# Kernel tuning notes

Measured on AMD Instinct MI355X. Metric: run time of the kernel, lower is better.

Reference implementation:

```python
import jax, jax.numpy as jnp
import numpy as np

B, N, T, F_IN, F_OUT = 4, 2048, 12, 32, 32
ALPHA = 0.2  # leaky relu negative slope
NEG_INF = -9e15


def setup_inputs() -> dict:
    key = jax.random.key(0)
    k = jax.random.split(key, 6)
    x = jax.random.normal(k[0], (B, N, T, F_IN), dtype=jnp.float32)
    adj = jax.random.randint(k[1], (N, N), 0, 2, dtype=jnp.int32)
    W = jax.random.normal(k[2], (T * F_IN, T * F_OUT), dtype=jnp.float32) * 0.05
    a = jax.random.normal(k[3], (2 * T * F_OUT, 1), dtype=jnp.float32) * 0.05
    conv_w = jax.random.normal(k[4], (T, T, 3), dtype=jnp.float32) * 0.1  # (out_ch, in_ch, k)
    conv_b = jnp.zeros((T,), dtype=jnp.float32)
    return {"x": x, "adj": adj, "W": W, "a": a, "conv_w": conv_w, "conv_b": conv_b}


def reference(x, adj, W, a, conv_w, conv_b):
    Bz, Nn, Tt, Fi = x.shape
    Fo = W.shape[1] // Tt
    # temporal conv: channels = timesteps, length = nodes*features
    xt = x.transpose(0, 2, 1, 3).reshape(Bz, Tt, Nn * Fi)  # (B,T,L)
    xt = jax.lax.conv_general_dilated(
        xt, conv_w, window_strides=(1,), padding=[(1, 1)],
        dimension_numbers=("NCH", "OIH", "NCH")) + conv_b[None, :, None]
    xt = xt.reshape(Bz, Tt, Nn, Fi).transpose(0, 2, 1, 3).reshape(Bz, Nn, Tt * Fi)
    Wh = xt @ W  # (B, N, T*Fo)
    # e[b,i,j] = leakyrelu(Wh[b,i].a1 + Wh[b,j].a2)  -- avoids O(N^2 * 2F) concat
    a1 = a[: Tt * Fo, 0]
    a2 = a[Tt * Fo:, 0]
    f1 = Wh @ a1  # (B, N)
    f2 = Wh @ a2  # (B, N)
    e = jax.nn.leaky_relu(f1[:, :, None] + f2[:, None, :], negative_slope=ALPHA)
    e = jnp.where(adj[None, :, :] > 0, e, NEG_INF)
    attn = jax.nn.softmax(e, axis=-1)  # (B, N, N); dropout omitted (eval mode)
    h_prime = attn @ Wh  # (B, N, T*Fo)
    return jax.nn.elu(h_prime).reshape(Bz, Nn, Tt, Fo)
```

## Files before the change

kernel.cpp:

```cpp
#include <hip/hip_runtime.h>

using short8 = __attribute__((ext_vector_type(8))) short;
using f32x4  = __attribute__((ext_vector_type(4))) float;
using f32x16 = __attribute__((ext_vector_type(16))) float;

__device__ __forceinline__ unsigned short f2bf(float f) {
  unsigned u = __float_as_uint(f);
  u += 0x7fffu + ((u >> 16) & 1u);
  return (unsigned short)(u >> 16);
}

__global__ __launch_bounds__(256) void pack_w_kernel(const float* __restrict__ W,
                                                     unsigned short* __restrict__ wtp) {
  const int f = blockIdx.x * 4 + (threadIdx.x >> 6);
  const int l = threadIdx.x & 63;
  const int kk = f / 24, ct = f % 24;
  const int il = l & 15, kg = l >> 4;
  const float* src = W + (size_t)(kk * 32 + kg * 8) * 384 + ct * 16 + il;
  short8 v;
#pragma unroll
  for (int e = 0; e < 8; ++e) v[e] = (short)f2bf(src[(size_t)e * 384]);
  *reinterpret_cast<short8*>((char*)wtp + ((size_t)f << 10) + l * 16) = v;
}

__global__ __launch_bounds__(256) void adjmask_kernel(const int* __restrict__ adj,
                                                      unsigned* __restrict__ adjm,
                                                      float* __restrict__ f12) {
  if (blockIdx.x < 64) f12[blockIdx.x * 256 + threadIdx.x] = 0.f;
  const int wv = (blockIdx.x << 2) + (threadIdx.x >> 6);
  const int lane = threadIdx.x & 63;
  const int row = wv >> 5, j0 = (wv & 31) << 6;
  unsigned long long mask = __ballot(adj[(size_t)row * 2048 + j0 + lane] > 0);
  if (lane == 0) {
    adjm[row * 64 + (j0 >> 5)]     = (unsigned)mask;
    adjm[row * 64 + (j0 >> 5) + 1] = (unsigned)(mask >> 32);
  }
}

__global__ __launch_bounds__(256) void gemm_wh5_kernel(const float* __restrict__ x,
                                                       const float* __restrict__ cw,
                                                       const float* __restrict__ cb,
                                                       const unsigned short* __restrict__ wtp,
                                                       const float* __restrict__ a,
                                                       unsigned short* __restrict__ whp,
                                                       float* __restrict__ f1,
                                                       float* __restrict__ f2) {
  __shared__ __align__(16) char lds[24768 + 6400 + 1792];
  float* xin = (float*)lds;
  unsigned short* atile = (unsigned short*)lds;
  unsigned short* wtile = (unsigned short*)(lds + 24768);
  float* cws = (float*)(lds + 24768 + 6400);
  float* cbs = cws + 432;

  const int tid = threadIdx.x;
  const int rb = blockIdx.x;
  const int b = rb >> 8;
  const int jg2 = (rb >> 1) & 127;
  const int ch2 = rb & 1;
  const int r0 = ((b << 7) + jg2) << 4;
  const int w = tid >> 6, lane = tid & 63;
  const int il = lane & 15, kg = lane >> 4;

  for (int i = tid; i < 432; i += 256) cws[i] = cw[i];
  if (tid < 12) cbs[tid] = cb[tid];
  const float* xb = x + (size_t)b * 2048 * 12 * 32;
#pragma unroll
  for (int t = 0; t < 12; ++t) {
    for (int i = tid; i < 514; i += 256) {
      const int gp = jg2 * 512 + i - 1;
      float v = 0.f;
      if ((unsigned)gp < 65536u) v = xb[((size_t)(gp >> 5) * 12 + t) * 32 + (gp & 31)];
      xin[t * 516 + i] = v;
    }
  }
  __syncthreads();

  const int ploc = tid * 2;
  float accv0[12], accv1[12];
#pragma unroll
  for (int to = 0; to < 12; ++to) { accv0[to] = cbs[to]; accv1[to] = cbs[to]; }
#pragma unroll
  for (int ti = 0; ti < 12; ++ti) {
    const float x0 = xin[ti * 516 + ploc];
    const float x1 = xin[ti * 516 + ploc + 1];
    const float x2 = xin[ti * 516 + ploc + 2];
    const float x3 = xin[ti * 516 + ploc + 3];
#pragma unroll
    for (int to = 0; to < 12; ++to) {
      const float* wp = &cws[(to * 12 + ti) * 3];
      const float w0 = wp[0], w1 = wp[1], w2 = wp[2];
      accv0[to] += x0 * w0 + x1 * w1 + x2 * w2;
      accv1[to] += x1 * w0 + x2 * w1 + x3 * w2;
    }
  }
  __syncthreads();

  {
    const int row = ploc >> 5, f = ploc & 31;
    unsigned* ap32 = (unsigned*)(atile + row * 392 + f);
#pragma unroll
    for (int to = 0; to < 12; ++to) {
      const unsigned lo = f2bf(accv0[to]), hi = f2bf(accv1[to]);
      ap32[to * 16] = lo | (hi << 16);
    }
  }
  __syncthreads();

  f32x4 acc[3];
#pragma unroll
  for (int t = 0; t < 3; ++t) acc[t] = (f32x4){0.f, 0.f, 0.f, 0.f};
  const unsigned short* arow = atile + il * 392 + kg * 8;
  const int ct0 = ch2 * 12 + w * 3;
  const char* wb = (const char*)wtp + ((size_t)ct0 << 10) + lane * 16;

  short8 bcur[3], bnxt[3];
#pragma unroll
  for (int t = 0; t < 3; ++t)
    bcur[t] = *reinterpret_cast<const short8*>(wb + ((size_t)t << 10));
#pragma unroll
  for (int kk = 0; kk < 12; ++kk) {
    if (kk < 11) {
#pragma unroll
      for (int t = 0; t < 3; ++t)
        bnxt[t] = *reinterpret_cast<const short8*>(wb + (((size_t)(kk + 1) * 24 + t) << 10));
    }
    short8 af = *reinterpret_cast<const short8*>(arow + kk * 32);
#pragma unroll
    for (int t = 0; t < 3; ++t)
      acc[t] = __builtin_amdgcn_mfma_f32_16x16x32_bf16(af, bcur[t], acc[t], 0, 0, 0);
#pragma unroll
    for (int t = 0; t < 3; ++t) bcur[t] = bnxt[t];
  }

  float p1[4] = {0.f, 0.f, 0.f, 0.f}, p2[4] = {0.f, 0.f, 0.f, 0.f};
#pragma unroll
  for (int t = 0; t < 3; ++t) {
    const int c = (ct0 + t) * 16 + il;
    const float a1v = a[c], a2v = a[384 + c];
#pragma unroll
    for (int r = 0; r < 4; ++r) { p1[r] += acc[t][r] * a1v; p2[r] += acc[t][r] * a2v; }
  }
#pragma unroll
  for (int off = 1; off < 16; off <<= 1) {
#pragma unroll
    for (int r = 0; r < 4; ++r) { p1[r] += __shfl_xor(p1[r], off); p2[r] += __shfl_xor(p2[r], off); }
  }
  if (il == 0) {
#pragma unroll
    for (int r = 0; r < 4; ++r) {
      atomicAdd(&f1[r0 + kg * 4 + r], p1[r]);
      atomicAdd(&f2[r0 + kg * 4 + r], p2[r]);
    }
  }
#pragma unroll
  for (int t = 0; t < 3; ++t)
#pragma unroll
    for (int r = 0; r < 4; ++r)
      wtile[(kg * 4 + r) * 200 + (w * 3 + t) * 16 + il] = f2bf(acc[t][r]);
  __syncthreads();

#pragma unroll
  for (int rep = 0; rep < 2; ++rep) {
    const int flat = rep * 256 + tid;
    if (flat < 384) {
      const int ct32l = flat >> 6, l = flat & 63;
      const int l5 = l & 31, hw2 = l >> 5;
      short8 v;
#pragma unroll
      for (int e = 0; e < 8; ++e)
        v[e] = (short)wtile[(hw2 * 8 + e) * 200 + ct32l * 32 + l5];
      const int ct32g = ch2 * 6 + ct32l;
      *reinterpret_cast<short8*>((char*)whp +
          ((((size_t)b * 128 + jg2) * 12 + ct32g) << 10) + l * 16) = v;
    }
  }
}

__global__ __launch_bounds__(256) void etab_kernel(const float* __restrict__ f2,
                                                   unsigned* __restrict__ etab) {
  const int b = blockIdx.x;
  const int tid = threadIdx.x;
  for (int i = tid; i < 2048; i += 256) {
    const float v = f2[b * 2048 + i];
    const unsigned e2 = f2bf(__expf(v));
    const unsigned q2 = f2bf(__expf(0.2f * v));
    etab[b * 2048 + i] = (e2 << 16) | q2;
  }
}

__global__ __launch_bounds__(256, 3) void attn17_kernel(const float* __restrict__ f1,
                                                        const unsigned* __restrict__ etab,
                                                        const unsigned* __restrict__ adjm,
                                                        const unsigned short* __restrict__ whp,
                                                        float* __restrict__ out) {
  __shared__ float red[4][32][64];
  __shared__ float dred[128];
  const int bi = blockIdx.x;
  const int combo = bi % 12;
  const int b  = combo & 3;
  const int ch = combo >> 2;
  const int i0 = (bi / 12) << 5;
  const int tid = threadIdx.x;
  const int ks = tid >> 6;
  const int lane = tid & 63;
  const int l5 = lane & 31, hw = lane >> 5;
  const int hw8 = hw * 8;
  const int ig = i0 + l5;

  const unsigned* adjr = adjm + (size_t)ig * 64 + ks * 16;
  const unsigned* etb = etab + b * 2048 + ks * 512 + hw8;
  const char* pbase = (const char*)whp +
      ((((size_t)b * 128 + ks * 32) * 12 + ch * 4) << 10) + lane * 16;

  const float f1v = f1[b * 2048 + ig];
  const float T = __expf(-f1v);
  const float R = __expf(-0.8f * f1v);

  const f32x16 zero16 = {0.f,0.f,0.f,0.f,0.f,0.f,0.f,0.f,0.f,0.f,0.f,0.f,0.f,0.f,0.f,0.f};
  f32x16 acc[4];
#pragma unroll
  for (int t = 0; t < 4; ++t) acc[t] = zero16;
  float denom = 0.f;

  short8 bA[4], bB[4];
  uint4 eA0, eA1, eB0, eB1;
  unsigned wC, wN;

#define LOADB(AR, KK)                                                                   \
  { _Pragma("unroll")                                                                   \
    for (int tt = 0; tt < 4; ++tt)                                                      \
      AR[tt] = *reinterpret_cast<const short8*>(pbase + (size_t)(KK) * 12288 +          \
                                                (size_t)tt * 1024); }

#define PELE(UW, BIT, DST)                                                              \
  { const float e2_ = __uint_as_float((UW) & 0xffff0000u);                              \
    const float q2_ = __uint_as_float((UW) << 16);                                      \
    const float v_ = (e2_ > T) ? e2_ : R * q2_;                                         \
    DST = ((bits_ >> (BIT)) & 1u) ? v_ : 0.f; }

#define PKBF(HI, LO) (((__float_as_uint(HI) + 0x8000u) & 0xffff0000u) |                 \
                      ((__float_as_uint(LO) + 0x8000u) >> 16))

#define STEPD(AR, T0, T1, SH, KK, DL)                                                   \
  { const unsigned bits_ = wC >> ((SH) + hw8);                                          \
    float p0_, p1_, p2_, p3_, p4_, p5_, p6_, p7_;                                       \
    PELE(T0.x, 0, p0_)  PELE(T0.y, 1, p1_)  PELE(T0.z, 2, p2_)  PELE(T0.w, 3, p3_)      \
    PELE(T1.x, 4, p4_)  PELE(T1.y, 5, p5_)  PELE(T1.z, 6, p6_)  PELE(T1.w, 7, p7_)      \
    denom += (((p0_ + p1_) + (p2_ + p3_)) + ((p4_ + p5_) + (p6_ + p7_)));               \
    union { unsigned u[4]; short8 s8; } cc;                                             \
    cc.u[0] = PKBF(p1_, p0_); cc.u[1] = PKBF(p3_, p2_);                                 \
    cc.u[2] = PKBF(p5_, p4_); cc.u[3] = PKBF(p7_, p6_);                                 \
    _Pragma("unroll")                                                                   \
    for (int tt = 0; tt < 4; ++tt)                                                      \
      acc[tt] = __builtin_amdgcn_mfma_f32_32x32x16_bf16(cc.s8, AR[tt], acc[tt], 0, 0, 0); \
    if (DL) {                                                                           \
      LOADB(AR, (KK) + 2)                                                               \
      const unsigned* ep_ = etb + ((KK) + 2) * 16;                                      \
      T0 = *reinterpret_cast<const uint4*>(ep_);                                        \
      T1 = *reinterpret_cast<const uint4*>(ep_ + 4);                                    \
    } }

  LOADB(bA, 0) LOADB(bB, 1)
  eA0 = *reinterpret_cast<const uint4*>(etb);
  eA1 = *reinterpret_cast<const uint4*>(etb + 4);
  eB0 = *reinterpret_cast<const uint4*>(etb + 16);
  eB1 = *reinterpret_cast<const uint4*>(etb + 20);
  wC = adjr[0];
  wN = adjr[1];

  for (int t = 0; t < 16; ++t) {
    STEPD(bA, eA0, eA1, 0, 2 * t, (t < 15))
    STEPD(bB, eB0, eB1, 16, 2 * t + 1, (t < 15))
    wC = wN;
    wN = adjr[(t + 2 < 16) ? t + 2 : 15];
  }
#undef LOADB
#undef PELE
#undef PKBF
#undef STEPD

  float dn = denom + __shfl_xor(denom, 32);
  if (hw == 0) dred[ks * 32 + l5] = dn;

#pragma unroll
  for (int r = 0; r < 2; ++r) {
#pragma unroll
    for (int tt = 0; tt < 2; ++tt) {
#pragma unroll
      for (int q = 0; q < 16; ++q) {
        const int row = (q & 3) + 8 * (q >> 2) + 4 * hw;
        red[ks][row][tt * 32 + l5] = acc[r * 2 + tt][q];
      }
    }
    __syncthreads();
    const size_t ob = ((size_t)b * 2048 + i0) * 384 + ch * 128 + r * 64;
#pragma unroll
    for (int p = 0; p < 8; ++p) {
      const int idx = p * 256 + tid;
      const int row = idx >> 6;
      const int c = idx & 63;
      float v = red[0][row][c] + red[1][row][c] + red[2][row][c] + red[3][row][c];
      const float d = dred[row] + dred[32 + row] + dred[64 + row] + dred[96 + row];
      v /= d;
      v = v > 0.f ? v : expm1f(v);
      out[ob + (size_t)row * 384 + c] = v;
    }
    __syncthreads();
  }
}

extern "C" void kernel_launch(void* const* d_in, const int* in_sizes, int n_in,
                              void* d_out, int out_size, void* d_ws, size_t ws_size,
                              hipStream_t stream) {
  const float* x  = (const float*)d_in[0];
  const int* adj  = (const int*)d_in[1];
  const float* W  = (const float*)d_in[2];
  const float* a  = (const float*)d_in[3];
  const float* cw = (const float*)d_in[4];
  const float* cb = (const float*)d_in[5];
  float* out = (float*)d_out;

  char* ws = (char*)d_ws;
  unsigned short* wtp = (unsigned short*)ws; ws += (size_t)147456 * 2;
  unsigned short* whp = (unsigned short*)ws; ws += (size_t)3145728 * 2;
  float* f1           = (float*)ws;          ws += (size_t)8192 * 4;
  float* f2           = (float*)ws;          ws += (size_t)8192 * 4;
  unsigned* adjm      = (unsigned*)ws;       ws += (size_t)2048 * 64 * 4;
  unsigned* etab      = (unsigned*)ws;       ws += (size_t)8192 * 4;

  pack_w_kernel<<<dim3(72), 256, 0, stream>>>(W, wtp);
  adjmask_kernel<<<dim3(16384), 256, 0, stream>>>(adj, adjm, f1);
  gemm_wh5_kernel<<<dim3(1024), 256, 0, stream>>>(x, cw, cb, wtp, a, whp, f1, f2);
  etab_kernel<<<dim3(4), 256, 0, stream>>>(f2, etab);
  attn17_kernel<<<dim3(768), 256, 0, stream>>>(f1, etab, adjm, whp, out);
}
```

Measured before the change: 78.63 us.

## Compute full output width per block in conv+GEMM kernel to avoid duplicate conv

The Wh GEMM kernel previously split the 384 output columns across two blocks, so each block recomputed the same temporal convolution and A-tile. Now one block covers all 24 column tiles (6 per wave), which halves the grid and removes the duplicated convolution and x loads. The f1/f2 partial sums are reduced in LDS and written directly instead of global atomics, so the zeroing in adjmask is dropped. The first W fragments are also prefetched before the barrier. The cost is more registers per wave, more LDS, and fewer blocks for latency hiding.

Measured after the change: 76.16 us (median of 2 runs). -3.1%, faster.

```diff
diff --git a/kernel.cpp b/kernel.cpp
--- a/kernel.cpp
+++ b/kernel.cpp
@@ -24,9 +24,7 @@
 }
 
 __global__ __launch_bounds__(256) void adjmask_kernel(const int* __restrict__ adj,
-                                                      unsigned* __restrict__ adjm,
-                                                      float* __restrict__ f12) {
-  if (blockIdx.x < 64) f12[blockIdx.x * 256 + threadIdx.x] = 0.f;
+                                                      unsigned* __restrict__ adjm) {
   const int wv = (blockIdx.x << 2) + (threadIdx.x >> 6);
   const int lane = threadIdx.x & 63;
   const int row = wv >> 5, j0 = (wv & 31) << 6;
@@ -37,7 +35,7 @@
   }
 }
 
-__global__ __launch_bounds__(256) void gemm_wh5_kernel(const float* __restrict__ x,
+__global__ __launch_bounds__(256) void gemm_wh6_kernel(const float* __restrict__ x,
                                                        const float* __restrict__ cw,
                                                        const float* __restrict__ cb,
                                                        const unsigned short* __restrict__ wtp,
@@ -45,24 +43,25 @@
                                                        unsigned short* __restrict__ whp,
                                                        float* __restrict__ f1,
                                                        float* __restrict__ f2) {
-  __shared__ __align__(16) char lds[24768 + 6400 + 1792];
+  __shared__ __align__(16) char lds[24768 + 12544 + 1792 + 128];
   float* xin = (float*)lds;
   unsigned short* atile = (unsigned short*)lds;
   unsigned short* wtile = (unsigned short*)(lds + 24768);
-  float* cws = (float*)(lds + 24768 + 6400);
+  float* cws = (float*)(lds + 24768 + 12544);
   float* cbs = cws + 432;
+  float* s1s = (float*)(lds + 24768 + 12544 + 1792);
+  float* s2s = s1s + 16;
 
   const int tid = threadIdx.x;
   const int rb = blockIdx.x;
-  const int b = rb >> 8;
-  const int jg2 = (rb >> 1) & 127;
-  const int ch2 = rb & 1;
-  const int r0 = ((b << 7) + jg2) << 4;
+  const int b = rb >> 7, jg2 = rb & 127;
+  const int r0 = rb << 4;
   const int w = tid >> 6, lane = tid & 63;
   const int il = lane & 15, kg = lane >> 4;
 
   for (int i = tid; i < 432; i += 256) cws[i] = cw[i];
   if (tid < 12) cbs[tid] = cb[tid];
+  if (tid < 16) { s1s[tid] = 0.f; s2s[tid] = 0.f; }
   const float* xb = x + (size_t)b * 2048 * 12 * 32;
 #pragma unroll
   for (int t = 0; t < 12; ++t) {
@@ -73,6 +72,14 @@
       xin[t * 516 + i] = v;
     }
   }
+
+  const int ct0 = w * 6;
+  const char* wb = (const char*)wtp + ((size_t)ct0 << 10) + lane * 16;
+  short8 bcur[6], bnxt[6];
+#pragma unroll
+  for (int t = 0; t < 6; ++t)
+    bcur[t] = *reinterpret_cast<const short8*>(wb + ((size_t)t << 10));
+
   __syncthreads();
 
   const int ploc = tid * 2;
@@ -106,35 +113,28 @@
   }
   __syncthreads();
 
-  f32x4 acc[3];
-#pragma unroll
-  for (int t = 0; t < 3; ++t) acc[t] = (f32x4){0.f, 0.f, 0.f, 0.f};
+  f32x4 acc[6];
+#pragma unroll
+  for (int t = 0; t < 6; ++t) acc[t] = (f32x4){0.f, 0.f, 0.f, 0.f};
   const unsigned short* arow = atile + il * 392 + kg * 8;
-  const int ct0 = ch2 * 12 + w * 3;
-  const char* wb = (const char*)wtp + ((size_t)ct0 << 10) + lane * 16;
-
-  short8 bcur[3], bnxt[3];
-#pragma unroll
-  for (int t = 0; t < 3; ++t)
-    bcur[t] = *reinterpret_cast<const short8*>(wb + ((size_t)t << 10));
 #pragma unroll
   for (int kk = 0; kk < 12; ++kk) {
     if (kk < 11) {
 #pragma unroll
-      for (int t = 0; t < 3; ++t)
+      for (int t = 0; t < 6; ++t)
         bnxt[t] = *reinterpret_cast<const short8*>(wb + (((size_t)(kk + 1) * 24 + t) << 10));
     }
     short8 af = *reinterpret_cast<const short8*>(arow + kk * 32);
 #pragma unroll
-    for (int t = 0; t < 3; ++t)
+    for (int t = 0; t < 6; ++t)
       acc[t] = __builtin_amdgcn_mfma_f32_16x16x32_bf16(af, bcur[t], acc[t], 0, 0, 0);
 #pragma unroll
-    for (int t = 0; t < 3; ++t) bcur[t] = bnxt[t];
+    for (int t = 0; t < 6; ++t) bcur[t] = bnxt[t];
   }
 
   float p1[4] = {0.f, 0.f, 0.f, 0.f}, p2[4] = {0.f, 0.f, 0.f, 0.f};
 #pragma unroll
-  for (int t = 0; t < 3; ++t) {
+  for (int t = 0; t < 6; ++t) {
     const int c = (ct0 + t) * 16 + il;
     const float a1v = a[c], a2v = a[384 + c];
 #pragma unroll
@@ -148,32 +148,30 @@
   if (il == 0) {
 #pragma unroll
     for (int r = 0; r < 4; ++r) {
-      atomicAdd(&f1[r0 + kg * 4 + r], p1[r]);
-      atomicAdd(&f2[r0 + kg * 4 + r], p2[r]);
-    }
-  }
-#pragma unroll
-  for (int t = 0; t < 3; ++t)
+      atomicAdd(&s1s[kg * 4 + r], p1[r]);
+      atomicAdd(&s2s[kg * 4 + r], p2[r]);
+    }
+  }
+#pragma unroll
+  for (int t = 0; t < 6; ++t)
 #pragma unroll
     for (int r = 0; r < 4; ++r)
-      wtile[(kg * 4 + r) * 200 + (w * 3 + t) * 16 + il] = f2bf(acc[t][r]);
+      wtile[(kg * 4 + r) * 392 + (ct0 + t) * 16 + il] = f2bf(acc[t][r]);
   __syncthreads();
 
 #pragma unroll
-  for (int rep = 0; rep < 2; ++rep) {
+  for (int rep = 0; rep < 3; ++rep) {
     const int flat = rep * 256 + tid;
-    if (flat < 384) {
-      const int ct32l = flat >> 6, l = flat & 63;
-      const int l5 = l & 31, hw2 = l >> 5;
-      short8 v;
-#pragma unroll
-      for (int e = 0; e < 8; ++e)
-        v[e] = (short)wtile[(hw2 * 8 + e) * 200 + ct32l * 32 + l5];
-      const int ct32g = ch2 * 6 + ct32l;
-      *reinterpret_cast<short8*>((char*)whp +
-          ((((size_t)b * 128 + jg2) * 12 + ct32g) << 10) + l * 16) = v;
-    }
-  }
+    const int ct32 = flat >> 6, l = flat & 63;
+    const int l5 = l & 31, hw2 = l >> 5;
+    short8 v;
+#pragma unroll
+    for (int e = 0; e < 8; ++e)
+      v[e] = (short)wtile[(hw2 * 8 + e) * 392 + ct32 * 32 + l5];
+    *reinterpret_cast<short8*>((char*)whp +
+        ((((size_t)b * 128 + jg2) * 12 + ct32) << 10) + l * 16) = v;
+  }
+  if (tid < 16) { f1[r0 + tid] = s1s[tid]; f2[r0 + tid] = s2s[tid]; }
 }
 
 __global__ __launch_bounds__(256) void etab_kernel(const float* __restrict__ f2,
@@ -329,8 +327,8 @@
   unsigned* etab      = (unsigned*)ws;       ws += (size_t)8192 * 4;
 
   pack_w_kernel<<<dim3(72), 256, 0, stream>>>(W, wtp);
-  adjmask_kernel<<<dim3(16384), 256, 0, stream>>>(adj, adjm, f1);
-  gemm_wh5_kernel<<<dim3(1024), 256, 0, stream>>>(x, cw, cb, wtp, a, whp, f1, f2);
+  adjmask_kernel<<<dim3(16384), 256, 0, stream>>>(adj, adjm);
+  gemm_wh6_kernel<<<dim3(512), 256, 0, stream>>>(x, cw, cb, wtp, a, whp, f1, f2);
   etab_kernel<<<dim3(4), 256, 0, stream>>>(f2, etab);
   attn17_kernel<<<dim3(768), 256, 0, stream>>>(f1, etab, adjm, whp, out);
 }
```

## Split temporal conv into its own kernel writing MFMA-packed bf16 operands

Applied to the files above, without the earlier changes.

Moves the temporal convolution out of the Wh GEMM kernel into a separate conv kernel that writes its bf16 output directly in the MFMA A-fragment layout to a new global buffer. The GEMM kernel then streams A fragments from global memory with register double-buffering instead of staging them through LDS. Before, each conv tile was computed twice, once for each of the two column-half blocks; now it is computed once. The cost is an extra kernel launch and a global write plus read of the 6 MB activation buffer.

Measured after the change: 83.34 us. 6.0% more time.

```diff
diff --git a/kernel.cpp b/kernel.cpp
--- a/kernel.cpp
+++ b/kernel.cpp
@@ -37,21 +37,71 @@
   }
 }
 
-__global__ __launch_bounds__(256) void gemm_wh5_kernel(const float* __restrict__ x,
-                                                       const float* __restrict__ cw,
-                                                       const float* __restrict__ cb,
+__global__ __launch_bounds__(256) void conv2_kernel(const float* __restrict__ x,
+                                                    const float* __restrict__ cw,
+                                                    const float* __restrict__ cb,
+                                                    unsigned short* __restrict__ atp) {
+  __shared__ __align__(16) char lds[24768 + 1792];
+  float* xin = (float*)lds;
+  float* cws = (float*)(lds + 24768);
+  float* cbs = cws + 432;
+
+  const int tid = threadIdx.x;
+  const int rb = blockIdx.x;
+  const int b = rb >> 7, jg2 = rb & 127;
+
+  for (int i = tid; i < 432; i += 256) cws[i] = cw[i];
+  if (tid < 12) cbs[tid] = cb[tid];
+  const float* xb = x + (size_t)b * 2048 * 12 * 32;
+#pragma unroll
+  for (int t = 0; t < 12; ++t) {
+    for (int i = tid; i < 514; i += 256) {
+      const int gp = jg2 * 512 + i - 1;
+      float v = 0.f;
+      if ((unsigned)gp < 65536u) v = xb[((size_t)(gp >> 5) * 12 + t) * 32 + (gp & 31)];
+      xin[t * 516 + i] = v;
+    }
+  }
+  __syncthreads();
+
+  const int ploc = tid * 2;
+  float accv0[12], accv1[12];
+#pragma unroll
+  for (int to = 0; to < 12; ++to) { accv0[to] = cbs[to]; accv1[to] = cbs[to]; }
+#pragma unroll
+  for (int ti = 0; ti < 12; ++ti) {
+    const float x0 = xin[ti * 516 + ploc];
+    const float x1 = xin[ti * 516 + ploc + 1];
+    const float x2 = xin[ti * 516 + ploc + 2];
+    const float x3 = xin[ti * 516 + ploc + 3];
+#pragma unroll
+    for (int to = 0; to < 12; ++to) {
+      const float* wp = &cws[(to * 12 + ti) * 3];
+      const float w0 = wp[0], w1 = wp[1], w2 = wp[2];
+      accv0[to] += x0 * w0 + x1 * w1 + x2 * w2;
+      accv1[to] += x1 * w0 + x2 * w1 + x3 * w2;
+    }
+  }
+
+  {
+    const int row = ploc >> 5, f = ploc & 31;
+    const int lane = (f >> 3) * 16 + row;
+    char* base = (char*)atp + (((size_t)(b * 128 + jg2) * 12) << 10) + lane * 16 + (f & 7) * 2;
+#pragma unroll
+    for (int to = 0; to < 12; ++to) {
+      const unsigned lo = f2bf(accv0[to]), hi = f2bf(accv1[to]);
+      *reinterpret_cast<unsigned*>(base + ((size_t)to << 10)) = lo | (hi << 16);
+    }
+  }
+}
+
+__global__ __launch_bounds__(256) void gemm_wh7_kernel(const unsigned short* __restrict__ atp,
                                                        const unsigned short* __restrict__ wtp,
                                                        const float* __restrict__ a,
                                                        unsigned short* __restrict__ whp,
                                                        float* __restrict__ f1,
                                                        float* __restrict__ f2) {
-  __shared__ __align__(16) char lds[24768 + 6400 + 1792];
-  float* xin = (float*)lds;
-  unsigned short* atile = (unsigned short*)lds;
-  unsigned short* wtile = (unsigned short*)(lds + 24768);
-  float* cws = (float*)(lds + 24768 + 6400);
-  float* cbs = cws + 432;
-
+  __shared__ unsigned short wtile[16][200];
   const int tid = threadIdx.x;
   const int rb = blockIdx.x;
   const int b = rb >> 8;
@@ -61,73 +111,32 @@
   const int w = tid >> 6, lane = tid & 63;
   const int il = lane & 15, kg = lane >> 4;
 
-  for (int i = tid; i < 432; i += 256) cws[i] = cw[i];
-  if (tid < 12) cbs[tid] = cb[tid];
-  const float* xb = x + (size_t)b * 2048 * 12 * 32;
-#pragma unroll
-  for (int t = 0; t < 12; ++t) {
-    for (int i = tid; i < 514; i += 256) {
-      const int gp = jg2 * 512 + i - 1;
-      float v = 0.f;
-      if ((unsigned)gp < 65536u) v = xb[((size_t)(gp >> 5) * 12 + t) * 32 + (gp & 31)];
-      xin[t * 516 + i] = v;
-    }
-  }
-  __syncthreads();
-
-  const int ploc = tid * 2;
-  float accv0[12], accv1[12];
-#pragma unroll
-  for (int to = 0; to < 12; ++to) { accv0[to] = cbs[to]; accv1[to] = cbs[to]; }
-#pragma unroll
-  for (int ti = 0; ti < 12; ++ti) {
-    const float x0 = xin[ti * 516 + ploc];
-    const float x1 = xin[ti * 516 + ploc + 1];
-    const float x2 = xin[ti * 516 + ploc + 2];
-    const float x3 = xin[ti * 516 + ploc + 3];
-#pragma unroll
-    for (int to = 0; to < 12; ++to) {
-      const float* wp = &cws[(to * 12 + ti) * 3];
-      const float w0 = wp[0], w1 = wp[1], w2 = wp[2];
-      accv0[to] += x0 * w0 + x1 * w1 + x2 * w2;
-      accv1[to] += x1 * w0 + x2 * w1 + x3 * w2;
-    }
-  }
-  __syncthreads();
-
-  {
-    const int row = ploc >> 5, f = ploc & 31;
-    unsigned* ap32 = (unsigned*)(atile + row * 392 + f);
-#pragma unroll
-    for (int to = 0; to < 12; ++to) {
-      const unsigned lo = f2bf(accv0[to]), hi = f2bf(accv1[to]);
-      ap32[to * 16] = lo | (hi << 16);
-    }
-  }
-  __syncthreads();
-
-  f32x4 acc[3];
-#pragma unroll
-  for (int t = 0; t < 3; ++t) acc[t] = (f32x4){0.f, 0.f, 0.f, 0.f};
-  const unsigned short* arow = atile + il * 392 + kg * 8;
+  const char* abase = (const char*)atp + (((size_t)(b * 128 + jg2) * 12) << 10) + lane * 16;
   const int ct0 = ch2 * 12 + w * 3;
   const char* wb = (const char*)wtp + ((size_t)ct0 << 10) + lane * 16;
 
-  short8 bcur[3], bnxt[3];
+  f32x4 acc[3];
+#pragma unroll
+  for (int t = 0; t < 3; ++t) acc[t] = (f32x4){0.f, 0.f, 0.f, 0.f};
+
+  short8 aC, aN, bcur[3], bnxt[3];
+  aC = *reinterpret_cast<const short8*>(abase);
 #pragma unroll
   for (int t = 0; t < 3; ++t)
     bcur[t] = *reinterpret_cast<const short8*>(wb + ((size_t)t << 10));
+
 #pragma unroll
   for (int kk = 0; kk < 12; ++kk) {
     if (kk < 11) {
+      aN = *reinterpret_cast<const short8*>(abase + ((size_t)(kk + 1) << 10));
 #pragma unroll
       for (int t = 0; t < 3; ++t)
         bnxt[t] = *reinterpret_cast<const short8*>(wb + (((size_t)(kk + 1) * 24 + t) << 10));
     }
-    short8 af = *reinterpret_cast<const short8*>(arow + kk * 32);
 #pragma unroll
     for (int t = 0; t < 3; ++t)
-      acc[t] = __builtin_amdgcn_mfma_f32_16x16x32_bf16(af, bcur[t], acc[t], 0, 0, 0);
+      acc[t] = __builtin_amdgcn_mfma_f32_16x16x32_bf16(aC, bcur[t], acc[t], 0, 0, 0);
+    aC = aN;
 #pragma unroll
     for (int t = 0; t < 3; ++t) bcur[t] = bnxt[t];
   }
@@ -156,7 +165,7 @@
   for (int t = 0; t < 3; ++t)
 #pragma unroll
     for (int r = 0; r < 4; ++r)
-      wtile[(kg * 4 + r) * 200 + (w * 3 + t) * 16 + il] = f2bf(acc[t][r]);
+      wtile[kg * 4 + r][(w * 3 + t) * 16 + il] = f2bf(acc[t][r]);
   __syncthreads();
 
 #pragma unroll
@@ -168,7 +177,7 @@
       short8 v;
 #pragma unroll
       for (int e = 0; e < 8; ++e)
-        v[e] = (short)wtile[(hw2 * 8 + e) * 200 + ct32l * 32 + l5];
+        v[e] = (short)wtile[hw2 * 8 + e][ct32l * 32 + l5];
       const int ct32g = ch2 * 6 + ct32l;
       *reinterpret_cast<short8*>((char*)whp +
           ((((size_t)b * 128 + jg2) * 12 + ct32g) << 10) + l * 16) = v;
@@ -322,6 +331,7 @@
 
   char* ws = (char*)d_ws;
   unsigned short* wtp = (unsigned short*)ws; ws += (size_t)147456 * 2;
+  unsigned short* atp = (unsigned short*)ws; ws += (size_t)3145728 * 2;
   unsigned short* whp = (unsigned short*)ws; ws += (size_t)3145728 * 2;
   float* f1           = (float*)ws;          ws += (size_t)8192 * 4;
   float* f2           = (float*)ws;          ws += (size_t)8192 * 4;
@@ -330,7 +340,8 @@
 
   pack_w_kernel<<<dim3(72), 256, 0, stream>>>(W, wtp);
   adjmask_kernel<<<dim3(16384), 256, 0, stream>>>(adj, adjm, f1);
-  gemm_wh5_kernel<<<dim3(1024), 256, 0, stream>>>(x, cw, cb, wtp, a, whp, f1, f2);
+  conv2_kernel<<<dim3(512), 256, 0, stream>>>(x, cw, cb, atp);
+  gemm_wh7_kernel<<<dim3(1024), 256, 0, stream>>>(atp, wtp, a, whp, f1, f2);
   etab_kernel<<<dim3(4), 256, 0, stream>>>(f2, etab);
   attn17_kernel<<<dim3(768), 256, 0, stream>>>(f1, etab, adjm, whp, out);
 }
```
